# Kernel tuning notes

Measured on AMD Instinct MI355X. Metric: run time of the kernel, lower is better.

Reference implementation:

```python
import jax, jax.numpy as jnp
import numpy as np

SCALE = 0.05  # temperature from the module
C, NUM, IN_DIM, HID = 64, 128, 768, 128


def _l2norm(x):
    n = jnp.sqrt(jnp.sum(x * x, axis=-1, keepdims=True))
    return x / jnp.maximum(n, 1e-12)


def setup_inputs() -> dict:
    key = jax.random.key(0)
    k1, k2, k3, k4 = jax.random.split(key, 4)
    embeds = jax.random.normal(k1, (C, NUM, IN_DIM), dtype=jnp.float32)
    head_w = jax.random.normal(k2, (HID, IN_DIM), dtype=jnp.float32) * (1.0 / np.sqrt(IN_DIM))
    head_b = jax.random.normal(k3, (HID,), dtype=jnp.float32) * 0.01
    proto = jax.random.normal(k4, (C, HID), dtype=jnp.float32) * (1.0 / np.sqrt(HID))
    return {"embeds": embeds, "head_w": head_w, "head_b": head_b, "proto": proto}


def reference(embeds, head_w, head_b, proto):
    # x = head(embeds): [C, num, hid]
    x = jnp.einsum('cni,hi->cnh', embeds, head_w) + head_b
    num = x.shape[1]
    num_classes = proto.shape[0]

    nx = _l2norm(x)            # [C, num, d]
    nproto = _l2norm(proto)    # [C, d]

    # ---- prototype contrastive term (loop over i in num, fused) ----
    # sim_mat[c, n, k] = exp(cos(x[c,n], proto[k]) / scale)
    sim_mat = jnp.exp(jnp.einsum('cnd,kd->cnk', nx, nproto) / SCALE)
    pos = jnp.diagonal(sim_mat, axis1=0, axis2=2)      # [num, C], pos[n,c] = sim_mat[c,n,c]
    total = sim_mat.sum(-1).T                           # [num, C]
    loss = -jnp.log(pos / total).sum()
    loss = loss / (num * num_classes * num_classes)

    # ---- instance-instance term (loop over i in num_classes, fused) ----
    # S[a, m, b, n] = exp(cos(x[a,m], x[b,n]) / scale)
    S = jnp.exp(jnp.einsum('amd,bnd->ambn', nx, nx) / SCALE)
    # per-anchor-class i: pos_ins[m, n] = S[i, m, i, n]
    pos_ins = jnp.diagonal(S, axis1=0, axis2=2)         # [m, n, C(i)]
    sumA = jnp.transpose(S.sum(0), (0, 2, 1))           # [m, n, C(i)]
    neg_ins = (sumA - pos_ins).sum(0)                   # [n, C(i)]
    loss_ins = -jnp.log(pos_ins / (pos_ins + neg_ins[None, :, :])).sum()
    loss_ins = loss_ins / (num * num_classes * num * num_classes)

    return loss + loss_ins
```

## Files before the change

kernel.cpp:

```cpp
#include <hip/hip_runtime.h>
#include <math.h>

#define SCALE_INV 20.0f
#define EXPK 28.853900817779268f
#define LN2F 0.6931471805599453f

typedef __bf16 bf16x8 __attribute__((ext_vector_type(8)));
typedef float  f32x4  __attribute__((ext_vector_type(4)));

__global__ __launch_bounds__(256) void k_headnorm(const float* __restrict__ e,
                                                  const float* __restrict__ w,
                                                  const float* __restrict__ hb,
                                                  __bf16* __restrict__ nxb,
                                                  __bf16* __restrict__ nxe,
                                                  float* __restrict__ cspart,
                                                  float* __restrict__ accs) {
  __shared__ __bf16 Ab[32 * 72];
  __shared__ __bf16 Bb[128 * 72];
  __shared__ float  xt[32 * 132];
  __shared__ float  hbl[128];
  const int t  = threadIdx.x;
  const int rt = blockIdx.x;
  if (t < 128) hbl[t] = hb[t];
  if (t < 32) cspart[rt * 32 + t] = 0.0f;
  if (rt == 0 && t >= 128 && t < 132) accs[t - 128] = 0.0f;

  const int arow = t >> 3, akoff = (t & 7) * 8;
  const int brow = t >> 1, bkoff = (t & 1) * 32;
  float4 ar[2], br[8];
  {
    const float* p = &e[(rt * 32 + arow) * 768 + akoff];
    ar[0] = *(const float4*)p; ar[1] = *(const float4*)(p + 4);
    const float* q = &w[brow * 768 + bkoff];
    for (int i = 0; i < 8; i++) br[i] = *(const float4*)(q + 4 * i);
  }

  const int wv = t >> 6, lane = t & 63;
  const int quad = lane >> 4, lrow = lane & 15;
  const int rb = wv & 1, cb = wv >> 1;
  f32x4 acc[4];
  f32x4 zero = {0.f, 0.f, 0.f, 0.f};
  for (int j = 0; j < 4; j++) acc[j] = zero;

  for (int it = 0; it < 12; it++) {
    {
      __bf16 ta[8];
      const float* f = (const float*)ar;
      for (int i = 0; i < 8; i++) ta[i] = (__bf16)f[i];
      *(bf16x8*)&Ab[arow * 72 + akoff] = *(bf16x8*)ta;
      const float* g = (const float*)br;
      for (int seg = 0; seg < 4; seg++) {
        __bf16 tb[8];
        for (int i = 0; i < 8; i++) tb[i] = (__bf16)g[seg * 8 + i];
        *(bf16x8*)&Bb[brow * 72 + bkoff + seg * 8] = *(bf16x8*)tb;
      }
    }
    __syncthreads();
    if (it < 11) {
      int kb = (it + 1) * 64;
      const float* p = &e[(rt * 32 + arow) * 768 + kb + akoff];
      ar[0] = *(const float4*)p; ar[1] = *(const float4*)(p + 4);
      const float* q = &w[brow * 768 + kb + bkoff];
      for (int i = 0; i < 8; i++) br[i] = *(const float4*)(q + 4 * i);
    }
    for (int kc = 0; kc < 2; kc++) {
      bf16x8 a = *(const bf16x8*)&Ab[(rb * 16 + lrow) * 72 + kc * 32 + quad * 8];
      for (int j = 0; j < 4; j++) {
        bf16x8 b = *(const bf16x8*)&Bb[(cb * 64 + j * 16 + lrow) * 72 + kc * 32 + quad * 8];
        acc[j] = __builtin_amdgcn_mfma_f32_16x16x32_bf16(a, b, acc[j], 0, 0, 0);
      }
    }
    __syncthreads();
  }

  for (int j = 0; j < 4; j++)
    for (int r = 0; r < 4; r++) {
      int row = rb * 16 + quad * 4 + r;
      int col = cb * 64 + j * 16 + lrow;
      xt[row * 132 + col] = acc[j][r] + hbl[col];
    }
  __syncthreads();
  {
    int row = t >> 3, c0 = (t & 7) * 16;
    float v[16];
    float s = 0.0f;
    for (int i = 0; i < 4; i++) {
      float4 f = *(const float4*)&xt[row * 132 + c0 + i * 4];
      v[i * 4] = f.x; v[i * 4 + 1] = f.y; v[i * 4 + 2] = f.z; v[i * 4 + 3] = f.w;
    }
    for (int i = 0; i < 16; i++) s += v[i] * v[i];
    s += __shfl_xor(s, 1, 64);
    s += __shfl_xor(s, 2, 64);
    s += __shfl_xor(s, 4, 64);
    float inv = 1.0f / fmaxf(sqrtf(s), 1e-12f);
    __bf16 o[16], oe[16];
    for (int i = 0; i < 16; i++) {
      float nv = v[i] * inv;
      o[i]  = (__bf16)nv;
      oe[i] = (__bf16)(nv * EXPK);
    }
    __bf16* dst = &nxb[(rt * 32 + row) * 128 + c0];
    *(bf16x8*)dst       = *(bf16x8*)o;
    *(bf16x8*)(dst + 8) = *(bf16x8*)(o + 8);
    __bf16* dse = &nxe[(rt * 32 + row) * 128 + c0];
    *(bf16x8*)dse       = *(bf16x8*)oe;
    *(bf16x8*)(dse + 8) = *(bf16x8*)(oe + 8);
  }
}

__global__ __launch_bounds__(256) void k_colsum(const __bf16* __restrict__ nxb,
                                                const __bf16* __restrict__ nxe,
                                                float* __restrict__ cspart) {
  __shared__ __bf16 At[128 * 136];
  __shared__ __bf16 Bt[128 * 136];
  __shared__ float  colpart[4 * 128];
  const int t    = threadIdx.x;
  const int cj   = blockIdx.x;
  const int rs   = blockIdx.y;
  const int w    = t >> 6, lane = t & 63;
  const int quad = lane >> 4, lrow = lane & 15;
  const int sr   = t >> 4, sseg = t & 15;

  for (int it = 0; it < 8; it++) {
    int r = sr + it * 16;
    *(bf16x8*)&Bt[r * 136 + sseg * 8] =
        *(const bf16x8*)&nxe[(cj * 128 + r) * 128 + sseg * 8];
  }
  int tiles[4], nt = 0;
  for (int mm = 0; mm < 4; mm++) {
    int m = rs * 4 + 1 + mm;
    if (m < 32 || cj < 32) tiles[nt++] = (cj + m) & 63;
  }
  bf16x8 pre[8];
  for (int it = 0; it < 8; it++)
    pre[it] = *(const bf16x8*)&nxb[(tiles[0] * 128 + sr + it * 16) * 128 + sseg * 8];

  float colacc[8];
  for (int j = 0; j < 8; j++) colacc[j] = 0.0f;

  for (int ti = 0; ti < nt; ti++) {
    const int ci = tiles[ti];
    for (int it = 0; it < 8; it++)
      *(bf16x8*)&At[(sr + it * 16) * 136 + sseg * 8] = pre[it];
    __syncthreads();
    if (ti + 1 < nt) {
      int cn = tiles[ti + 1];
      for (int it = 0; it < 8; it++)
        pre[it] = *(const bf16x8*)&nxb[(cn * 128 + sr + it * 16) * 128 + sseg * 8];
    }
    f32x4 acc[2][8];
    f32x4 zero = {0.0f, 0.0f, 0.0f, 0.0f};
    for (int i = 0; i < 2; i++)
      for (int j = 0; j < 8; j++) acc[i][j] = zero;
    for (int kc = 0; kc < 4; kc++) {
      bf16x8 a0 = *(const bf16x8*)&At[(w * 32 + lrow) * 136 + kc * 32 + quad * 8];
      bf16x8 a1 = *(const bf16x8*)&At[(w * 32 + 16 + lrow) * 136 + kc * 32 + quad * 8];
      for (int j = 0; j < 8; j++) {
        bf16x8 b = *(const bf16x8*)&Bt[(j * 16 + lrow) * 136 + kc * 32 + quad * 8];
        acc[0][j] = __builtin_amdgcn_mfma_f32_16x16x32_bf16(a0, b, acc[0][j], 0, 0, 0);
        acc[1][j] = __builtin_amdgcn_mfma_f32_16x16x32_bf16(a1, b, acc[1][j], 0, 0, 0);
      }
    }
    float rsum[2][4];
    for (int i = 0; i < 2; i++)
      for (int r = 0; r < 4; r++) rsum[i][r] = 0.0f;
    for (int i = 0; i < 2; i++)
      for (int j = 0; j < 8; j++)
        for (int r = 0; r < 4; r++) {
          float ev = exp2f(acc[i][j][r]);
          colacc[j]  += ev;
          rsum[i][r] += ev;
        }
    for (int i = 0; i < 2; i++)
      for (int r = 0; r < 4; r++) {
        float v = rsum[i][r];
        v += __shfl_xor(v, 1, 64);
        v += __shfl_xor(v, 2, 64);
        v += __shfl_xor(v, 4, 64);
        v += __shfl_xor(v, 8, 64);
        if (lrow == 0)
          atomicAdd(&cspart[ci * 128 + w * 32 + i * 16 + quad * 4 + r], v);
      }
    __syncthreads();
  }

  for (int j = 0; j < 8; j++) {
    float v = colacc[j];
    v += __shfl_xor(v, 16, 64);
    v += __shfl_xor(v, 32, 64);
    if (lane < 16) colpart[w * 128 + j * 16 + lane] = v;
  }
  __syncthreads();
  if (t < 128) {
    float s = colpart[t] + colpart[128 + t] + colpart[256 + t] + colpart[384 + t];
    atomicAdd(&cspart[cj * 128 + t], s);
  }
}

__global__ __launch_bounds__(256) void k_fused(const __bf16* __restrict__ nxb,
                                               const __bf16* __restrict__ nxe,
                                               const float* __restrict__ proto,
                                               const float* __restrict__ cspart,
                                               float* __restrict__ accs,
                                               float* __restrict__ out) {
  __shared__ __bf16 Xt[64 * 136];
  __shared__ __bf16 XtE[128 * 136];
  __shared__ __bf16 PtE[64 * 136];
  __shared__ float  negl[128];
  const int t = threadIdx.x, cls = blockIdx.x, half = blockIdx.y;
  const int sr = t >> 4, sseg = t & 15;

  {
    const int rw = t >> 2, part = t & 3;
    float v[32];
    float s = 0.0f;
    const float* p = &proto[rw * 128 + part * 32];
    for (int i = 0; i < 8; i++) {
      float4 f = *(const float4*)(p + 4 * i);
      v[i * 4] = f.x; v[i * 4 + 1] = f.y; v[i * 4 + 2] = f.z; v[i * 4 + 3] = f.w;
      s += f.x * f.x + f.y * f.y + f.z * f.z + f.w * f.w;
    }
    s += __shfl_xor(s, 1, 64);
    s += __shfl_xor(s, 2, 64);
    float inv = EXPK / fmaxf(sqrtf(s), 1e-12f);
    __bf16 o[32];
    for (int i = 0; i < 32; i++) o[i] = (__bf16)(v[i] * inv);
    __bf16* dst = &PtE[rw * 136 + part * 32];
    for (int i = 0; i < 4; i++) *(bf16x8*)(dst + i * 8) = *(bf16x8*)(o + i * 8);
  }
  for (int it = 0; it < 4; it++) {
    int r = sr + it * 16;
    *(bf16x8*)&Xt[r * 136 + sseg * 8] =
        *(const bf16x8*)&nxb[(cls * 128 + half * 64 + r) * 128 + sseg * 8];
  }
  for (int it = 0; it < 8; it++) {
    int r = sr + it * 16;
    *(bf16x8*)&XtE[r * 136 + sseg * 8] =
        *(const bf16x8*)&nxe[(cls * 128 + r) * 128 + sseg * 8];
  }
  if (t < 128) negl[t] = cspart[cls * 128 + t];
  __syncthreads();

  const int wv = t >> 6, lane = t & 63;
  const int quad = lane >> 4, lrow = lane & 15;
  f32x4 zero = {0.f, 0.f, 0.f, 0.f};
  f32x4 acc_i[8], acc_p[4];
  for (int j = 0; j < 8; j++) acc_i[j] = zero;
  for (int j = 0; j < 4; j++) acc_p[j] = zero;

  for (int kc = 0; kc < 4; kc++) {
    bf16x8 a = *(const bf16x8*)&Xt[(wv * 16 + lrow) * 136 + kc * 32 + quad * 8];
    for (int j = 0; j < 8; j++) {
      bf16x8 b = *(const bf16x8*)&XtE[(j * 16 + lrow) * 136 + kc * 32 + quad * 8];
      acc_i[j] = __builtin_amdgcn_mfma_f32_16x16x32_bf16(a, b, acc_i[j], 0, 0, 0);
    }
    for (int j = 0; j < 4; j++) {
      bf16x8 b = *(const bf16x8*)&PtE[(j * 16 + lrow) * 136 + kc * 32 + quad * 8];
      acc_p[j] = __builtin_amdgcn_mfma_f32_16x16x32_bf16(a, b, acc_p[j], 0, 0, 0);
    }
  }

  float wacc0 = 0.0f;
  for (int r = 0; r < 4; r++) {
    float tot = 0.0f;
    for (int j = 0; j < 4; j++) tot += exp2f(acc_p[j][r]);
    tot += __shfl_xor(tot, 1, 64);
    tot += __shfl_xor(tot, 2, 64);
    tot += __shfl_xor(tot, 4, 64);
    tot += __shfl_xor(tot, 8, 64);
    if (lrow == 0) wacc0 += logf(tot);
  }
  {
    const int jc = cls >> 4, colc = cls & 15;
    if (lrow == colc) {
      float sd = 0.0f;
      switch (jc) {
        case 0: for (int r = 0; r < 4; r++) sd += acc_p[0][r]; break;
        case 1: for (int r = 0; r < 4; r++) sd += acc_p[1][r]; break;
        case 2: for (int r = 0; r < 4; r++) sd += acc_p[2][r]; break;
        default: for (int r = 0; r < 4; r++) sd += acc_p[3][r]; break;
      }
      wacc0 -= sd * LN2F;
    }
  }
  float wacc1 = 0.0f;
  for (int j = 0; j < 8; j++) {
    float ng = negl[j * 16 + lrow];
    for (int r = 0; r < 4; r++)
      wacc1 += log1pf(ng * exp2f(-acc_i[j][r]));
  }
  for (int off = 32; off; off >>= 1) {
    wacc0 += __shfl_xor(wacc0, off, 64);
    wacc1 += __shfl_xor(wacc1, off, 64);
  }
  if (lane == 0) {
    atomicAdd(&accs[0], wacc0);
    atomicAdd(&accs[1], wacc1);
  }
  __syncthreads();
  if (t == 0) {
    __threadfence();
    unsigned int old = atomicAdd((unsigned int*)&accs[2], 1u);
    if (old == 127u) {
      __threadfence();
      float a0 = atomicAdd(&accs[0], 0.0f);
      float a1 = atomicAdd(&accs[1], 0.0f);
      out[0] = a0 * (1.0f / 524288.0f) + a1 * (1.0f / 67108864.0f);
    }
  }
}

extern "C" void kernel_launch(void* const* d_in, const int* in_sizes, int n_in,
                              void* d_out, int out_size, void* d_ws, size_t ws_size,
                              hipStream_t stream) {
  const float* e  = (const float*)d_in[0];
  const float* w  = (const float*)d_in[1];
  const float* hb = (const float*)d_in[2];
  const float* pr = (const float*)d_in[3];
  char* ws = (char*)d_ws;
  __bf16* nxb    = (__bf16*)ws;
  __bf16* nxe    = (__bf16*)(ws + (2 << 20));
  float*  cspart = (float*)(ws + (4 << 20));
  float*  accs   = (float*)(ws + (4 << 20) + (64 << 10));
  float*  out    = (float*)d_out;

  k_headnorm<<<256, 256, 0, stream>>>(e, w, hb, nxb, nxe, cspart, accs);
  k_colsum<<<dim3(64, 8), 256, 0, stream>>>(nxb, nxe, cspart);
  k_fused<<<dim3(64, 2), 256, 0, stream>>>(nxb, nxe, pr, cspart, accs, out);
}
```

Baseline: 142.0 us.

## Move diagonal and prototype GEMMs into colsum grid, add light final reduction kernel

Adds two extra rows of blocks to the colsum grid. One row computes each class's diagonal self-similarity block and writes the raw logits to a workspace buffer. The other row computes the prototype contrastive term. The old fused kernel is replaced by a lightweight kernel that streams those stored logits and applies log1p with the column sums, so the diagonal GEMM overlaps with the column-sum work. The trade-off is an extra 4 MB fp32 write and read, and a new counter slot, accs[3], which must be zeroed by the head kernel (not visible here).

```diff
diff --git a/kernel.cpp b/kernel.cpp
--- a/kernel.cpp
+++ b/kernel.cpp
@@ -110,7 +110,10 @@
 
 __global__ __launch_bounds__(256) void k_colsum(const __bf16* __restrict__ nxb,
                                                 const __bf16* __restrict__ nxe,
-                                                float* __restrict__ cspart) {
+                                                const float* __restrict__ proto,
+                                                float* __restrict__ cspart,
+                                                float* __restrict__ posD,
+                                                float* __restrict__ accs) {
   __shared__ __bf16 At[128 * 136];
   __shared__ __bf16 Bt[128 * 136];
   __shared__ float  colpart[4 * 128];
@@ -121,33 +124,90 @@
   const int quad = lane >> 4, lrow = lane & 15;
   const int sr   = t >> 4, sseg = t & 15;
 
-  for (int it = 0; it < 8; it++) {
-    int r = sr + it * 16;
-    *(bf16x8*)&Bt[r * 136 + sseg * 8] =
-        *(const bf16x8*)&nxe[(cj * 128 + r) * 128 + sseg * 8];
-  }
-  int tiles[4], nt = 0;
-  for (int mm = 0; mm < 4; mm++) {
-    int m = rs * 4 + 1 + mm;
-    if (m < 32 || cj < 32) tiles[nt++] = (cj + m) & 63;
-  }
-  bf16x8 pre[8];
-  for (int it = 0; it < 8; it++)
-    pre[it] = *(const bf16x8*)&nxb[(tiles[0] * 128 + sr + it * 16) * 128 + sseg * 8];
-
-  float colacc[8];
-  for (int j = 0; j < 8; j++) colacc[j] = 0.0f;
-
-  for (int ti = 0; ti < nt; ti++) {
-    const int ci = tiles[ti];
+  if (rs < 8) {
+    for (int it = 0; it < 8; it++) {
+      int r = sr + it * 16;
+      *(bf16x8*)&Bt[r * 136 + sseg * 8] =
+          *(const bf16x8*)&nxe[(cj * 128 + r) * 128 + sseg * 8];
+    }
+    int tiles[4], nt = 0;
+    for (int mm = 0; mm < 4; mm++) {
+      int m = rs * 4 + 1 + mm;
+      if (m < 32 || cj < 32) tiles[nt++] = (cj + m) & 63;
+    }
+    bf16x8 pre[8];
     for (int it = 0; it < 8; it++)
-      *(bf16x8*)&At[(sr + it * 16) * 136 + sseg * 8] = pre[it];
-    __syncthreads();
-    if (ti + 1 < nt) {
-      int cn = tiles[ti + 1];
+      pre[it] = *(const bf16x8*)&nxb[(tiles[0] * 128 + sr + it * 16) * 128 + sseg * 8];
+
+    float colacc[8];
+    for (int j = 0; j < 8; j++) colacc[j] = 0.0f;
+
+    for (int ti = 0; ti < nt; ti++) {
+      const int ci = tiles[ti];
       for (int it = 0; it < 8; it++)
-        pre[it] = *(const bf16x8*)&nxb[(cn * 128 + sr + it * 16) * 128 + sseg * 8];
-    }
+        *(bf16x8*)&At[(sr + it * 16) * 136 + sseg * 8] = pre[it];
+      __syncthreads();
+      if (ti + 1 < nt) {
+        int cn = tiles[ti + 1];
+        for (int it = 0; it < 8; it++)
+          pre[it] = *(const bf16x8*)&nxb[(cn * 128 + sr + it * 16) * 128 + sseg * 8];
+      }
+      f32x4 acc[2][8];
+      f32x4 zero = {0.0f, 0.0f, 0.0f, 0.0f};
+      for (int i = 0; i < 2; i++)
+        for (int j = 0; j < 8; j++) acc[i][j] = zero;
+      for (int kc = 0; kc < 4; kc++) {
+        bf16x8 a0 = *(const bf16x8*)&At[(w * 32 + lrow) * 136 + kc * 32 + quad * 8];
+        bf16x8 a1 = *(const bf16x8*)&At[(w * 32 + 16 + lrow) * 136 + kc * 32 + quad * 8];
+        for (int j = 0; j < 8; j++) {
+          bf16x8 b = *(const bf16x8*)&Bt[(j * 16 + lrow) * 136 + kc * 32 + quad * 8];
+          acc[0][j] = __builtin_amdgcn_mfma_f32_16x16x32_bf16(a0, b, acc[0][j], 0, 0, 0);
+          acc[1][j] = __builtin_amdgcn_mfma_f32_16x16x32_bf16(a1, b, acc[1][j], 0, 0, 0);
+        }
+      }
+      float rsum[2][4];
+      for (int i = 0; i < 2; i++)
+        for (int r = 0; r < 4; r++) rsum[i][r] = 0.0f;
+      for (int i = 0; i < 2; i++)
+        for (int j = 0; j < 8; j++)
+          for (int r = 0; r < 4; r++) {
+            float ev = exp2f(acc[i][j][r]);
+            colacc[j]  += ev;
+            rsum[i][r] += ev;
+          }
+      for (int i = 0; i < 2; i++)
+        for (int r = 0; r < 4; r++) {
+          float v = rsum[i][r];
+          v += __shfl_xor(v, 1, 64);
+          v += __shfl_xor(v, 2, 64);
+          v += __shfl_xor(v, 4, 64);
+          v += __shfl_xor(v, 8, 64);
+          if (lrow == 0)
+            atomicAdd(&cspart[ci * 128 + w * 32 + i * 16 + quad * 4 + r], v);
+        }
+      __syncthreads();
+    }
+
+    for (int j = 0; j < 8; j++) {
+      float v = colacc[j];
+      v += __shfl_xor(v, 16, 64);
+      v += __shfl_xor(v, 32, 64);
+      if (lane < 16) colpart[w * 128 + j * 16 + lane] = v;
+    }
+    __syncthreads();
+    if (t < 128) {
+      float s = colpart[t] + colpart[128 + t] + colpart[256 + t] + colpart[384 + t];
+      atomicAdd(&cspart[cj * 128 + t], s);
+    }
+  } else if (rs == 8) {
+    for (int it = 0; it < 8; it++) {
+      int r = sr + it * 16;
+      *(bf16x8*)&At[r * 136 + sseg * 8] =
+          *(const bf16x8*)&nxb[(cj * 128 + r) * 128 + sseg * 8];
+      *(bf16x8*)&Bt[r * 136 + sseg * 8] =
+          *(const bf16x8*)&nxe[(cj * 128 + r) * 128 + sseg * 8];
+    }
+    __syncthreads();
     f32x4 acc[2][8];
     f32x4 zero = {0.0f, 0.0f, 0.0f, 0.0f};
     for (int i = 0; i < 2; i++)
@@ -161,147 +221,108 @@
         acc[1][j] = __builtin_amdgcn_mfma_f32_16x16x32_bf16(a1, b, acc[1][j], 0, 0, 0);
       }
     }
-    float rsum[2][4];
-    for (int i = 0; i < 2; i++)
-      for (int r = 0; r < 4; r++) rsum[i][r] = 0.0f;
     for (int i = 0; i < 2; i++)
       for (int j = 0; j < 8; j++)
         for (int r = 0; r < 4; r++) {
-          float ev = exp2f(acc[i][j][r]);
-          colacc[j]  += ev;
-          rsum[i][r] += ev;
+          int row = w * 32 + i * 16 + quad * 4 + r;
+          int col = j * 16 + lrow;
+          posD[cj * 16384 + row * 128 + col] = acc[i][j][r];
         }
+  } else {
+    for (int it = 0; it < 8; it++) {
+      int r = sr + it * 16;
+      *(bf16x8*)&At[r * 136 + sseg * 8] =
+          *(const bf16x8*)&nxb[(cj * 128 + r) * 128 + sseg * 8];
+    }
+    {
+      const int rw = t >> 2, part = t & 3;
+      float v[32];
+      float s = 0.0f;
+      const float* p = &proto[rw * 128 + part * 32];
+      for (int i = 0; i < 8; i++) {
+        float4 f = *(const float4*)(p + 4 * i);
+        v[i * 4] = f.x; v[i * 4 + 1] = f.y; v[i * 4 + 2] = f.z; v[i * 4 + 3] = f.w;
+        s += f.x * f.x + f.y * f.y + f.z * f.z + f.w * f.w;
+      }
+      s += __shfl_xor(s, 1, 64);
+      s += __shfl_xor(s, 2, 64);
+      float inv = EXPK / fmaxf(sqrtf(s), 1e-12f);
+      __bf16 o[32];
+      for (int i = 0; i < 32; i++) o[i] = (__bf16)(v[i] * inv);
+      __bf16* dst = &Bt[rw * 136 + part * 32];
+      for (int i = 0; i < 4; i++) *(bf16x8*)(dst + i * 8) = *(bf16x8*)(o + i * 8);
+    }
+    __syncthreads();
+    f32x4 acc_p[2][4];
+    f32x4 zero = {0.0f, 0.0f, 0.0f, 0.0f};
     for (int i = 0; i < 2; i++)
+      for (int j = 0; j < 4; j++) acc_p[i][j] = zero;
+    for (int kc = 0; kc < 4; kc++) {
+      bf16x8 a0 = *(const bf16x8*)&At[(w * 32 + lrow) * 136 + kc * 32 + quad * 8];
+      bf16x8 a1 = *(const bf16x8*)&At[(w * 32 + 16 + lrow) * 136 + kc * 32 + quad * 8];
+      for (int j = 0; j < 4; j++) {
+        bf16x8 b = *(const bf16x8*)&Bt[(j * 16 + lrow) * 136 + kc * 32 + quad * 8];
+        acc_p[0][j] = __builtin_amdgcn_mfma_f32_16x16x32_bf16(a0, b, acc_p[0][j], 0, 0, 0);
+        acc_p[1][j] = __builtin_amdgcn_mfma_f32_16x16x32_bf16(a1, b, acc_p[1][j], 0, 0, 0);
+      }
+    }
+    float wacc0 = 0.0f;
+    for (int i = 0; i < 2; i++) {
       for (int r = 0; r < 4; r++) {
-        float v = rsum[i][r];
-        v += __shfl_xor(v, 1, 64);
-        v += __shfl_xor(v, 2, 64);
-        v += __shfl_xor(v, 4, 64);
-        v += __shfl_xor(v, 8, 64);
-        if (lrow == 0)
-          atomicAdd(&cspart[ci * 128 + w * 32 + i * 16 + quad * 4 + r], v);
-      }
-    __syncthreads();
-  }
-
-  for (int j = 0; j < 8; j++) {
-    float v = colacc[j];
-    v += __shfl_xor(v, 16, 64);
-    v += __shfl_xor(v, 32, 64);
-    if (lane < 16) colpart[w * 128 + j * 16 + lane] = v;
-  }
-  __syncthreads();
-  if (t < 128) {
-    float s = colpart[t] + colpart[128 + t] + colpart[256 + t] + colpart[384 + t];
-    atomicAdd(&cspart[cj * 128 + t], s);
+        float tot = 0.0f;
+        for (int j = 0; j < 4; j++) tot += exp2f(acc_p[i][j][r]);
+        tot += __shfl_xor(tot, 1, 64);
+        tot += __shfl_xor(tot, 2, 64);
+        tot += __shfl_xor(tot, 4, 64);
+        tot += __shfl_xor(tot, 8, 64);
+        if (lrow == 0) wacc0 += logf(tot);
+      }
+      const int jc = cj >> 4, colc = cj & 15;
+      if (lrow == colc) {
+        float sd = 0.0f;
+        switch (jc) {
+          case 0: for (int r = 0; r < 4; r++) sd += acc_p[i][0][r]; break;
+          case 1: for (int r = 0; r < 4; r++) sd += acc_p[i][1][r]; break;
+          case 2: for (int r = 0; r < 4; r++) sd += acc_p[i][2][r]; break;
+          default: for (int r = 0; r < 4; r++) sd += acc_p[i][3][r]; break;
+        }
+        wacc0 -= sd * LN2F;
+      }
+    }
+    for (int off = 32; off; off >>= 1) wacc0 += __shfl_xor(wacc0, off, 64);
+    if (lane == 0) atomicAdd(&accs[0], wacc0);
   }
 }
 
-__global__ __launch_bounds__(256) void k_fused(const __bf16* __restrict__ nxb,
-                                               const __bf16* __restrict__ nxe,
-                                               const float* __restrict__ proto,
-                                               const float* __restrict__ cspart,
-                                               float* __restrict__ accs,
-                                               float* __restrict__ out) {
-  __shared__ __bf16 Xt[64 * 136];
-  __shared__ __bf16 XtE[128 * 136];
-  __shared__ __bf16 PtE[64 * 136];
-  __shared__ float  negl[128];
-  const int t = threadIdx.x, cls = blockIdx.x, half = blockIdx.y;
-  const int sr = t >> 4, sseg = t & 15;
-
-  {
-    const int rw = t >> 2, part = t & 3;
-    float v[32];
-    float s = 0.0f;
-    const float* p = &proto[rw * 128 + part * 32];
-    for (int i = 0; i < 8; i++) {
-      float4 f = *(const float4*)(p + 4 * i);
-      v[i * 4] = f.x; v[i * 4 + 1] = f.y; v[i * 4 + 2] = f.z; v[i * 4 + 3] = f.w;
-      s += f.x * f.x + f.y * f.y + f.z * f.z + f.w * f.w;
-    }
-    s += __shfl_xor(s, 1, 64);
-    s += __shfl_xor(s, 2, 64);
-    float inv = EXPK / fmaxf(sqrtf(s), 1e-12f);
-    __bf16 o[32];
-    for (int i = 0; i < 32; i++) o[i] = (__bf16)(v[i] * inv);
-    __bf16* dst = &PtE[rw * 136 + part * 32];
-    for (int i = 0; i < 4; i++) *(bf16x8*)(dst + i * 8) = *(bf16x8*)(o + i * 8);
-  }
-  for (int it = 0; it < 4; it++) {
-    int r = sr + it * 16;
-    *(bf16x8*)&Xt[r * 136 + sseg * 8] =
-        *(const bf16x8*)&nxb[(cls * 128 + half * 64 + r) * 128 + sseg * 8];
-  }
-  for (int it = 0; it < 8; it++) {
-    int r = sr + it * 16;
-    *(bf16x8*)&XtE[r * 136 + sseg * 8] =
-        *(const bf16x8*)&nxe[(cls * 128 + r) * 128 + sseg * 8];
-  }
+__global__ __launch_bounds__(256) void k_last(const float* __restrict__ posD,
+                                              const float* __restrict__ cspart,
+                                              float* __restrict__ accs,
+                                              float* __restrict__ out) {
+  __shared__ float negl[128];
+  __shared__ float wred[4];
+  const int b = blockIdx.x, t = threadIdx.x;
+  const int cls = b >> 2, m0 = (b & 3) * 32;
   if (t < 128) negl[t] = cspart[cls * 128 + t];
   __syncthreads();
-
-  const int wv = t >> 6, lane = t & 63;
-  const int quad = lane >> 4, lrow = lane & 15;
-  f32x4 zero = {0.f, 0.f, 0.f, 0.f};
-  f32x4 acc_i[8], acc_p[4];
-  for (int j = 0; j < 8; j++) acc_i[j] = zero;
-  for (int j = 0; j < 4; j++) acc_p[j] = zero;
-
-  for (int kc = 0; kc < 4; kc++) {
-    bf16x8 a = *(const bf16x8*)&Xt[(wv * 16 + lrow) * 136 + kc * 32 + quad * 8];
-    for (int j = 0; j < 8; j++) {
-      bf16x8 b = *(const bf16x8*)&XtE[(j * 16 + lrow) * 136 + kc * 32 + quad * 8];
-      acc_i[j] = __builtin_amdgcn_mfma_f32_16x16x32_bf16(a, b, acc_i[j], 0, 0, 0);
-    }
-    for (int j = 0; j < 4; j++) {
-      bf16x8 b = *(const bf16x8*)&PtE[(j * 16 + lrow) * 136 + kc * 32 + quad * 8];
-      acc_p[j] = __builtin_amdgcn_mfma_f32_16x16x32_bf16(a, b, acc_p[j], 0, 0, 0);
-    }
-  }
-
-  float wacc0 = 0.0f;
-  for (int r = 0; r < 4; r++) {
-    float tot = 0.0f;
-    for (int j = 0; j < 4; j++) tot += exp2f(acc_p[j][r]);
-    tot += __shfl_xor(tot, 1, 64);
-    tot += __shfl_xor(tot, 2, 64);
-    tot += __shfl_xor(tot, 4, 64);
-    tot += __shfl_xor(tot, 8, 64);
-    if (lrow == 0) wacc0 += logf(tot);
-  }
-  {
-    const int jc = cls >> 4, colc = cls & 15;
-    if (lrow == colc) {
-      float sd = 0.0f;
-      switch (jc) {
-        case 0: for (int r = 0; r < 4; r++) sd += acc_p[0][r]; break;
-        case 1: for (int r = 0; r < 4; r++) sd += acc_p[1][r]; break;
-        case 2: for (int r = 0; r < 4; r++) sd += acc_p[2][r]; break;
-        default: for (int r = 0; r < 4; r++) sd += acc_p[3][r]; break;
-      }
-      wacc0 -= sd * LN2F;
-    }
-  }
-  float wacc1 = 0.0f;
-  for (int j = 0; j < 8; j++) {
-    float ng = negl[j * 16 + lrow];
-    for (int r = 0; r < 4; r++)
-      wacc1 += log1pf(ng * exp2f(-acc_i[j][r]));
-  }
-  for (int off = 32; off; off >>= 1) {
-    wacc0 += __shfl_xor(wacc0, off, 64);
-    wacc1 += __shfl_xor(wacc1, off, 64);
-  }
-  if (lane == 0) {
-    atomicAdd(&accs[0], wacc0);
-    atomicAdd(&accs[1], wacc1);
-  }
+  const float* base = &posD[cls * 16384 + m0 * 128];
+  float wacc = 0.0f;
+  for (int it = 0; it < 4; it++) {
+    int idx = (it * 256 + t) * 4;
+    float4 d = *(const float4*)&base[idx];
+    int n = idx & 127;
+    wacc += log1pf(negl[n]     * exp2f(-d.x));
+    wacc += log1pf(negl[n + 1] * exp2f(-d.y));
+    wacc += log1pf(negl[n + 2] * exp2f(-d.z));
+    wacc += log1pf(negl[n + 3] * exp2f(-d.w));
+  }
+  for (int off = 32; off; off >>= 1) wacc += __shfl_xor(wacc, off, 64);
+  if ((t & 63) == 0) wred[t >> 6] = wacc;
   __syncthreads();
   if (t == 0) {
+    atomicAdd(&accs[1], wred[0] + wred[1] + wred[2] + wred[3]);
     __threadfence();
-    unsigned int old = atomicAdd((unsigned int*)&accs[2], 1u);
-    if (old == 127u) {
+    unsigned int old = atomicAdd((unsigned int*)&accs[3], 1u);
+    if (old == 255u) {
       __threadfence();
       float a0 = atomicAdd(&accs[0], 0.0f);
       float a1 = atomicAdd(&accs[1], 0.0f);
@@ -322,9 +343,10 @@
   __bf16* nxe    = (__bf16*)(ws + (2 << 20));
   float*  cspart = (float*)(ws + (4 << 20));
   float*  accs   = (float*)(ws + (4 << 20) + (64 << 10));
+  float*  posD   = (float*)(ws + (5 << 20));
   float*  out    = (float*)d_out;
 
   k_headnorm<<<256, 256, 0, stream>>>(e, w, hb, nxb, nxe, cspart, accs);
-  k_colsum<<<dim3(64, 8), 256, 0, stream>>>(nxb, nxe, cspart);
-  k_fused<<<dim3(64, 2), 256, 0, stream>>>(nxb, nxe, pr, cspart, accs, out);
+  k_colsum<<<dim3(64, 10), 256, 0, stream>>>(nxb, nxe, pr, cspart, posD, accs);
+  k_last<<<256, 256, 0, stream>>>(posD, cspart, accs, out);
 }
```

Result: faster. 131.4 us (-7.5%).
